# Kernel optimization log

Measured on AMD Instinct MI355X. Metric: run time of the kernel, lower is better.

Reference implementation:

```python
import jax, jax.numpy as jnp
import numpy as np

B, S, H, L, C = 32, 512, 768, 512, 3  # batch, seq, hidden, max_length, num_classes


def _lin_init(k, fan_in, shape):
    return jax.random.normal(k, shape, jnp.float32) * (1.0 / np.sqrt(fan_in))


def setup_inputs() -> dict:
    key = jax.random.key(0)
    ks = jax.random.split(key, 18)
    return {
        "tokens": jax.random.normal(ks[0], (B, S, H), jnp.float32),
        # shared Q/K/V projections (used for both token- and feature-attention)
        "Wq": _lin_init(ks[1], H, (H, H)), "bq": jnp.zeros((H,), jnp.float32),
        "Wk": _lin_init(ks[2], H, (H, H)), "bk": jnp.zeros((H,), jnp.float32),
        "Wv": _lin_init(ks[3], H, (H, H)), "bv": jnp.zeros((H,), jnp.float32),
        # TSGSA: Linear(H,1)+ReLU gate over tokens
        "W_ts": _lin_init(ks[4], H, (H, 1)), "b_ts": jnp.zeros((1,), jnp.float32),
        # FSGSA: Linear(max_length,1)+ReLU gate over padded seq axis (also reused for FGSA per source bug)
        "W_fs": _lin_init(ks[5], L, (L, 1)), "b_fs": jnp.zeros((1,), jnp.float32),
        # TGSA: Linear(H,H)+Sigmoid gate
        "W_tg": _lin_init(ks[6], H, (H, H)), "b_tg": jnp.zeros((H,), jnp.float32),
        # fnn: Linear(7H,H) -> Linear(H,C)
        "W1": _lin_init(ks[7], 7 * H, (7 * H, H)), "b1": jnp.zeros((H,), jnp.float32),
        "W2": _lin_init(ks[8], H, (H, C)), "b2": jnp.zeros((C,), jnp.float32),
    }


def _ln(x):
    # LayerNorm over (seq, hidden) jointly, eps=1e-8; freshly-instantiated affine params are identity
    m = jnp.mean(x, axis=(1, 2), keepdims=True)
    v = jnp.var(x, axis=(1, 2), keepdims=True)
    return (x - m) * jax.lax.rsqrt(v + 1e-8)


def reference(tokens, Wq, bq, Wk, bk, Wv, bv, W_ts, b_ts, W_fs, b_fs, W_tg, b_tg, W1, b1, W2, b2):
    scale = 1.0 / np.sqrt(H)
    Q = tokens @ Wq + bq  # [B,S,H]
    K = tokens @ Wk + bk
    V = tokens @ Wv + bv
    # token-direction self-attention: softmax(Q K^T / sqrt(H)) V
    att = jax.nn.softmax(jnp.einsum('bsh,bth->bst', Q, K) * scale, axis=-1)  # [B,S,S]
    TSA = jnp.einsum('bst,bth->bsh', att, V)
    # feature-direction self-attention: V @ softmax(Q^T K / sqrt(H))
    attN = jax.nn.softmax(jnp.einsum('bsh,bsg->bhg', Q, K) * scale, axis=-1)  # [B,H,H]
    FSA = jnp.einsum('bsh,bhg->bsg', V, attN)
    # gate branches
    TSGSA = jax.nn.relu(tokens @ W_ts + b_ts) * tokens  # [B,S,1]*[B,S,H]
    tpad = jnp.pad(tokens.transpose(0, 2, 1), ((0, 0), (0, 0), (0, L - S)))  # [B,H,L]
    gate_f = jax.nn.relu(tpad @ W_fs + b_fs)  # [B,H,1]
    FSGSA = (gate_f * tokens.transpose(0, 2, 1)).transpose(0, 2, 1)  # [B,S,H]
    TGSA = jax.nn.sigmoid(tokens @ W_tg + b_tg) * tokens
    FGSA = FSGSA  # source bug: FGSA branch applies self.FSGSA, identical to FSGSA
    out_all = jnp.concatenate(
        [tokens, _ln(TSA), _ln(FSA), _ln(TGSA), _ln(FGSA), _ln(TSGSA), _ln(FSGSA)], axis=2)  # [B,S,7H]
    pooled = jnp.mean(out_all, axis=1)  # [B,7H]
    return (pooled @ W1 + b1) @ W2 + b2  # [B,C]
```

## Files before the change

kernel.cpp:

```cpp
#include <hip/hip_runtime.h>
#include <cmath>

typedef unsigned short u16;
typedef __attribute__((ext_vector_type(4))) float f32x4;
typedef __attribute__((ext_vector_type(4))) unsigned int u32x4;
typedef __attribute__((ext_vector_type(8))) __bf16 bf16x8;

__device__ __forceinline__ u16 f2b(float f) {
  unsigned int u = __builtin_bit_cast(unsigned int, f);
  return (u16)((u + 0x7fffu + ((u >> 16) & 1u)) >> 16);
}
__device__ __forceinline__ float b2f(u16 h) {
  unsigned int u = ((unsigned int)h) << 16;
  return __builtin_bit_cast(float, u);
}

__device__ __forceinline__ void glds16(const u16* g, u16* l) {
  __builtin_amdgcn_global_load_lds(
      (const __attribute__((address_space(1))) void*)g,
      (__attribute__((address_space(3))) void*)l, 16, 0, 0);
}

template <int EPI>
__global__ __launch_bounds__(256) void gemm_f_k(
    const u16* __restrict__ Ap, const u16* __restrict__ Bp, u16* __restrict__ Cp,
    u16* __restrict__ CpT, const float* __restrict__ bias,
    const float* __restrict__ tokp, float* __restrict__ colsum,
    float* __restrict__ bstat, int K, int lda, int ldb, int ldc, long sA,
    long sB, long sC, float scale) {
  __shared__ alignas(16) u16 smem[4][4096];

  const int gx = gridDim.x, gxy = gx * gridDim.y;
  const int nwg = gxy * gridDim.z;
  int orig = (blockIdx.z * gridDim.y + blockIdx.y) * gx + blockIdx.x;
  int gwi = (orig & 7) * (nwg >> 3) + (orig >> 3);
  const int z = gwi / gxy;
  int rem = gwi - z * gxy;
  const int ty = rem / gx, tx = rem - ty * gx;
  const int tileM = ty << 7, tileN = tx << 7;

  const u16* Abase = Ap + (size_t)z * sA;
  const u16* Bbase = Bp + (size_t)z * sB;

  const int tid = threadIdx.x;
  const int lane = tid & 63, w = tid >> 6;
  const int wr = (w >> 1) << 6, wc = (w & 1) << 6;
  const int fr = lane & 15, fg = lane >> 4;

  f32x4 acc[4][4];
#pragma unroll
  for (int i = 0; i < 4; ++i)
#pragma unroll
    for (int j = 0; j < 4; ++j) acc[i][j] = (f32x4){0.f, 0.f, 0.f, 0.f};

  const int srow = (w << 5) + (lane >> 2), scol = (lane & 3) << 3;
  const u16* gA = Abase + (size_t)(tileM + srow) * lda + scol;
  const u16* gB = Bbase + (size_t)(tileN + srow) * ldb + scol;
  const int ldsw = (w << 5) * 32;

  auto STAGE = [&](int buf, int k0) {
    const u16* ga = gA + k0;
    const u16* gb = gB + k0;
    u16* la = &smem[buf * 2][ldsw];
    u16* lb = &smem[buf * 2 + 1][ldsw];
    glds16(ga, la);
    glds16(ga + (size_t)16 * lda, la + 512);
    glds16(gb, lb);
    glds16(gb + (size_t)16 * ldb, lb + 512);
  };

  const int nt = K >> 5;
  STAGE(0, 0);
  int cur = 0;
  for (int t = 0; t < nt; ++t) {
    if (t + 1 < nt) {
      STAGE(cur ^ 1, (t + 1) << 5);
      asm volatile("s_waitcnt vmcnt(4)" ::: "memory");
    } else {
      asm volatile("s_waitcnt vmcnt(0)" ::: "memory");
    }
    __builtin_amdgcn_s_barrier();
    asm volatile("" ::: "memory");
    const u16* Ab = smem[cur * 2];
    const u16* Bb = smem[cur * 2 + 1];
    bf16x8 av[4], bw[4];
#pragma unroll
    for (int m = 0; m < 4; ++m)
      av[m] = *(const bf16x8*)&Ab[(wr + (m << 4) + fr) * 32 + (fg << 3)];
#pragma unroll
    for (int n = 0; n < 4; ++n)
      bw[n] = *(const bf16x8*)&Bb[(wc + (n << 4) + fr) * 32 + (fg << 3)];
#pragma unroll
    for (int m = 0; m < 4; ++m)
#pragma unroll
      for (int n = 0; n < 4; ++n)
        acc[m][n] =
            __builtin_amdgcn_mfma_f32_16x16x32_bf16(av[m], bw[n], acc[m][n], 0, 0, 0);
    asm volatile("" ::: "memory");
    __builtin_amdgcn_s_barrier();
    cur ^= 1;
  }

  if constexpr (EPI == 0 || EPI == 2) {
#pragma unroll
    for (int m = 0; m < 4; ++m) {
#pragma unroll
      for (int n = 0; n < 4; ++n) {
        const int gcol = tileN + wc + (n << 4) + fr;
#pragma unroll
        for (int r = 0; r < 4; ++r) {
          const int grow = tileM + wr + (m << 4) + (fg << 2) + r;
          float v = acc[m][n][r];
          if constexpr (EPI == 0) v += bias[gcol];
          else v *= scale;
          Cp[(size_t)z * sC + (size_t)grow * ldc + gcol] = f2b(v);
        }
      }
    }
    if constexpr (EPI == 0) {
      if (CpT) {
#pragma unroll
        for (int m = 0; m < 4; ++m) {
#pragma unroll
          for (int n = 0; n < 4; ++n) {
            const int gcol = tileN + wc + (n << 4) + fr;
            const int grow0 = tileM + wr + (m << 4) + (fg << 2);
            union { u16 u[4]; unsigned long long q; } pk;
#pragma unroll
            for (int r = 0; r < 4; ++r) pk.u[r] = f2b(acc[m][n][r] + bias[gcol]);
            *(unsigned long long*)&CpT[(size_t)gcol * 16384 + grow0] = pk.q;
          }
        }
      }
    }
  } else {
    __shared__ float scol_s[128];
    __shared__ float sred[2];
    if (tid < 128) scol_s[tid] = 0.f;
    if (tid == 0) { sred[0] = 0.f; sred[1] = 0.f; }
    __syncthreads();
    float ls = 0.f, lq = 0.f;
#pragma unroll
    for (int n = 0; n < 4; ++n) {
      float cpart = 0.f;
      const int gcol = tileN + wc + (n << 4) + fr;
#pragma unroll
      for (int m = 0; m < 4; ++m) {
#pragma unroll
        for (int r = 0; r < 4; ++r) {
          float v = acc[m][n][r];
          if constexpr (EPI == 1) {
            const int grow = tileM + wr + (m << 4) + (fg << 2) + r;
            float pre = v + bias[gcol];
            float g = 1.f / (1.f + __expf(-pre));
            v = g * tokp[(size_t)grow * 768 + gcol];
          }
          cpart += v; ls += v; lq += v * v;
        }
      }
      atomicAdd(&scol_s[wc + (n << 4) + fr], cpart);
    }
    atomicAdd(&sred[0], ls);
    atomicAdd(&sred[1], lq);
    __syncthreads();
    const int b = (EPI == 1) ? (tileM >> 9) : z;
    if (tid < 128) atomicAdd(&colsum[(size_t)b * 768 + tileN + tid], scol_s[tid]);
    if (tid == 0) {
      atomicAdd(&bstat[b], sred[0]);
      atomicAdd(&bstat[32 + b], sred[1]);
    }
  }
}

__global__ __launch_bounds__(256) void cvt_tok_k(const float* __restrict__ in,
                                                 u16* __restrict__ out) {
  const size_t i = ((size_t)blockIdx.x * 256 + threadIdx.x) * 8;
  f32x4 a = *(const f32x4*)(in + i), b = *(const f32x4*)(in + i + 4);
  union { u16 u[8]; u32x4 q; } pk;
#pragma unroll
  for (int j = 0; j < 4; ++j) { pk.u[j] = f2b(a[j]); pk.u[4 + j] = f2b(b[j]); }
  *(u32x4*)(out + i) = pk.q;
}

__global__ __launch_bounds__(256) void transpose_w_k(const float* __restrict__ W,
                                                     u16* __restrict__ WT) {
  __shared__ float t[64][65];
  const int r0 = blockIdx.y << 6, c0 = blockIdx.x << 6;
  for (int i = threadIdx.x; i < 4096; i += 256) {
    int r = i >> 6, c = i & 63;
    t[r][c] = W[(size_t)(r0 + r) * 768 + c0 + c];
  }
  __syncthreads();
  for (int i = threadIdx.x; i < 4096; i += 256) {
    int rr = i >> 6, cc = i & 63;
    WT[(size_t)(c0 + rr) * 768 + r0 + cc] = f2b(t[cc][rr]);
  }
}

__global__ __launch_bounds__(256) void transpose_bf_k(const u16* __restrict__ in,
                                                      u16* __restrict__ out) {
  __shared__ u16 t[64][72];
  const size_t base = (size_t)blockIdx.z * 589824;
  const int r0 = blockIdx.y << 6, c0 = blockIdx.x << 6;
  for (int i = threadIdx.x; i < 512; i += 256) {
    int r = i >> 3, c8 = (i & 7) << 3;
    union { u32x4 q; u16 u[8]; } pk;
    pk.q = *(const u32x4*)&in[base + (size_t)(r0 + r) * 768 + c0 + c8];
#pragma unroll
    for (int j = 0; j < 8; ++j) t[c8 + j][r] = pk.u[j];
  }
  __syncthreads();
  for (int i = threadIdx.x; i < 512; i += 256) {
    int r = i >> 3, c8 = (i & 7) << 3;
    *(u32x4*)&out[base + (size_t)(c0 + r) * 768 + r0 + c8] = *(u32x4*)&t[r][c8];
  }
}

template <int LEN>
__global__ __launch_bounds__(256) void softmax_k(u16* __restrict__ data) {
  constexpr int NP = LEN / 256;
  const int row = blockIdx.x, tid = threadIdx.x;
  u16* p = data + (size_t)row * LEN;
  const int lane = tid & 63, wid = tid >> 6;
  float v[NP];
  float mx = -1e30f;
#pragma unroll
  for (int i = 0; i < NP; ++i) { v[i] = b2f(p[tid + (i << 8)]); mx = fmaxf(mx, v[i]); }
#pragma unroll
  for (int o = 32; o > 0; o >>= 1) mx = fmaxf(mx, __shfl_xor(mx, o));
  __shared__ float red[4], red2[4];
  if (lane == 0) red[wid] = mx;
  __syncthreads();
  mx = fmaxf(fmaxf(red[0], red[1]), fmaxf(red[2], red[3]));
  float sum = 0.f;
#pragma unroll
  for (int i = 0; i < NP; ++i) { v[i] = __expf(v[i] - mx); sum += v[i]; }
#pragma unroll
  for (int o = 32; o > 0; o >>= 1) sum += __shfl_xor(sum, o);
  if (lane == 0) red2[wid] = sum;
  __syncthreads();
  sum = red2[0] + red2[1] + red2[2] + red2[3];
  const float inv = 1.f / sum;
#pragma unroll
  for (int i = 0; i < NP; ++i) p[tid + (i << 8)] = f2b(v[i] * inv);
}

__global__ __launch_bounds__(256) void row_stats_k(
    const float* __restrict__ tok, const float* __restrict__ Wts,
    const float* __restrict__ bts, float* __restrict__ gate_t,
    float* __restrict__ rowsum, float* __restrict__ rowsumsq) {
  const int wid = threadIdx.x >> 6, lane = threadIdx.x & 63;
  const int row = blockIdx.x * 4 + wid;
  const float* p = tok + (size_t)row * 768;
  float s = 0.f, q = 0.f, g = 0.f;
#pragma unroll
  for (int i = 0; i < 12; ++i) {
    float t = p[lane + i * 64];
    s += t; q += t * t; g += t * Wts[lane + i * 64];
  }
#pragma unroll
  for (int o = 32; o > 0; o >>= 1) {
    s += __shfl_xor(s, o); q += __shfl_xor(q, o); g += __shfl_xor(g, o);
  }
  if (lane == 0) {
    gate_t[row] = fmaxf(g + bts[0], 0.f);
    rowsum[row] = s;
    rowsumsq[row] = q;
  }
}

__global__ __launch_bounds__(256) void col_stats_k(
    const float* __restrict__ tok, const float* __restrict__ Wfs,
    const float* __restrict__ bfs, const float* __restrict__ gate_t,
    float* __restrict__ gate_f, float* __restrict__ colsum_tok,
    float* __restrict__ colsumsq_tok, float* __restrict__ colsum_tsg) {
  const int b = blockIdx.x, h = blockIdx.y * 256 + threadIdx.x;
  const float* p = tok + (size_t)b * 512 * 768 + h;
  const float* gt = gate_t + b * 512;
  float cs = 0.f, cq = 0.f, gf = 0.f, tg = 0.f;
#pragma unroll 4
  for (int s = 0; s < 512; ++s) {
    float t = p[(size_t)s * 768];
    cs += t; cq += t * t; gf += t * Wfs[s]; tg += t * gt[s];
  }
  const int idx = b * 768 + h;
  gate_f[idx] = fmaxf(gf + bfs[0], 0.f);
  colsum_tok[idx] = cs;
  colsumsq_tok[idx] = cq;
  colsum_tsg[idx] = tg;
}

__global__ __launch_bounds__(256) void batch_stats_k(
    const float* __restrict__ gate_t, const float* __restrict__ rowsum,
    const float* __restrict__ rowsumsq, const float* __restrict__ gate_f,
    const float* __restrict__ colsum_tok, const float* __restrict__ colsumsq_tok,
    float* __restrict__ st) {
  __shared__ float red[4][256];
  const int b = blockIdx.x, tid = threadIdx.x;
  float ts = 0.f, tq = 0.f, fs = 0.f, fq = 0.f;
  for (int s = tid; s < 512; s += 256) {
    float g = gate_t[b * 512 + s];
    ts += g * rowsum[b * 512 + s];
    tq += g * g * rowsumsq[b * 512 + s];
  }
  for (int h = tid; h < 768; h += 256) {
    float g = gate_f[b * 768 + h];
    fs += g * colsum_tok[b * 768 + h];
    fq += g * g * colsumsq_tok[b * 768 + h];
  }
  red[0][tid] = ts; red[1][tid] = tq; red[2][tid] = fs; red[3][tid] = fq;
  __syncthreads();
  for (int o = 128; o > 0; o >>= 1) {
    if (tid < o) {
      red[0][tid] += red[0][tid + o];
      red[1][tid] += red[1][tid + o];
      red[2][tid] += red[2][tid + o];
      red[3][tid] += red[3][tid + o];
    }
    __syncthreads();
  }
  if (tid == 0) {
    st[b] = red[0][0]; st[32 + b] = red[1][0];
    st[64 + b] = red[2][0]; st[96 + b] = red[3][0];
  }
}

__global__ __launch_bounds__(768) void pooled_k(
    const float* __restrict__ colsum_tok, const float* __restrict__ colsum_tsa,
    const float* __restrict__ bstat_tsa, const float* __restrict__ colsum_fsa,
    const float* __restrict__ bstat_fsa, const float* __restrict__ colsum_tgsa,
    const float* __restrict__ bstat_tgsa, const float* __restrict__ colsum_tsg,
    const float* __restrict__ gate_f, const float* __restrict__ st,
    float* __restrict__ pooled) {
  const int b = blockIdx.x, h = threadIdx.x;
  const float invS = 1.f / 512.f, invN = 1.f / (512.f * 768.f);
  const int i = b * 768 + h;
  float* pr = pooled + (size_t)b * 5376;
  pr[h] = colsum_tok[i] * invS;
  auto lnslot = [&](int slot, float cs, float bs, float bq) {
    float m = bs * invN;
    float var = bq * invN - m * m;
    pr[slot * 768 + h] = (cs * invS - m) * rsqrtf(var + 1e-8f);
  };
  lnslot(1, colsum_tsa[i], bstat_tsa[b], bstat_tsa[32 + b]);
  lnslot(2, colsum_fsa[i], bstat_fsa[b], bstat_fsa[32 + b]);
  lnslot(3, colsum_tgsa[i], bstat_tgsa[b], bstat_tgsa[32 + b]);
  const float fsg_cs = gate_f[i] * colsum_tok[i];
  lnslot(4, fsg_cs, st[64 + b], st[96 + b]);
  lnslot(5, colsum_tsg[i], st[b], st[32 + b]);
  lnslot(6, fsg_cs, st[64 + b], st[96 + b]);
}

__global__ __launch_bounds__(256) void fnn1_k(const float* __restrict__ pooled,
                                              const float* __restrict__ W1,
                                              float* __restrict__ tmp1) {
  __shared__ float sp[128][36];
  const int c0 = blockIdx.x << 7, k0 = blockIdx.y << 7;
  const int tid = threadIdx.x;
  for (int i = tid; i < 4096; i += 256) {
    int b = i >> 7, j = i & 127;
    sp[j][b] = pooled[(size_t)b * 5376 + k0 + j];
  }
  __syncthreads();
  const int c = c0 + (tid & 127);
  const int u = (tid >> 7) << 4;
  float acc[16];
#pragma unroll
  for (int t = 0; t < 16; ++t) acc[t] = 0.f;
#pragma unroll 4
  for (int j = 0; j < 128; ++j) {
    float w = W1[(size_t)(k0 + j) * 768 + c];
    const f32x4* row = (const f32x4*)&sp[j][u];
#pragma unroll
    for (int t4 = 0; t4 < 4; ++t4) {
      f32x4 v = row[t4];
#pragma unroll
      for (int r = 0; r < 4; ++r) acc[t4 * 4 + r] += v[r] * w;
    }
  }
#pragma unroll
  for (int t = 0; t < 16; ++t) atomicAdd(&tmp1[(u + t) * 768 + c], acc[t]);
}

__global__ __launch_bounds__(256) void fnn2_k(const float* __restrict__ tmp1,
                                              const float* __restrict__ b1,
                                              const float* __restrict__ W2,
                                              const float* __restrict__ b2,
                                              float* __restrict__ out) {
  const int gw = blockIdx.x * 4 + (threadIdx.x >> 6);
  const int lane = threadIdx.x & 63;
  const int b = gw / 3, c = gw % 3;
  float a = 0.f;
#pragma unroll
  for (int i = 0; i < 12; ++i) {
    int k = lane + i * 64;
    a += (tmp1[b * 768 + k] + b1[k]) * W2[k * 3 + c];
  }
#pragma unroll
  for (int o = 32; o > 0; o >>= 1) a += __shfl_xor(a, o);
  if (lane == 0) out[b * 3 + c] = a + b2[c];
}

extern "C" void kernel_launch(void* const* d_in, const int* in_sizes, int n_in,
                              void* d_out, int out_size, void* d_ws, size_t ws_size,
                              hipStream_t stream) {
  const float* tokens = (const float*)d_in[0];
  const float* Wq = (const float*)d_in[1];
  const float* bq = (const float*)d_in[2];
  const float* Wk = (const float*)d_in[3];
  const float* bk = (const float*)d_in[4];
  const float* Wv = (const float*)d_in[5];
  const float* bv = (const float*)d_in[6];
  const float* Wts = (const float*)d_in[7];
  const float* bts = (const float*)d_in[8];
  const float* Wfs = (const float*)d_in[9];
  const float* bfs = (const float*)d_in[10];
  const float* Wtg = (const float*)d_in[11];
  const float* btg = (const float*)d_in[12];
  const float* W1 = (const float*)d_in[13];
  const float* b1 = (const float*)d_in[14];
  const float* W2 = (const float*)d_in[15];
  const float* b2 = (const float*)d_in[16];
  float* out = (float*)d_out;

  char* ws = (char*)d_ws;
  size_t off = 0;
  auto take = [&](size_t bytes) -> char* {
    char* p = ws + off;
    off += (bytes + 255) & ~(size_t)255;
    return p;
  };
  u16* tokb = (u16*)take((size_t)16384 * 768 * 2);
  u16* WqT = (u16*)take((size_t)768 * 768 * 2);
  u16* WkT = (u16*)take((size_t)768 * 768 * 2);
  u16* WvT = (u16*)take((size_t)768 * 768 * 2);
  u16* WtgT = (u16*)take((size_t)768 * 768 * 2);
  u16* Qb = (u16*)take((size_t)16384 * 768 * 2);
  u16* Kb = (u16*)take((size_t)16384 * 768 * 2);
  u16* Vb = (u16*)take((size_t)16384 * 768 * 2);
  u16* Qt = (u16*)take((size_t)768 * 16384 * 2);
  u16* Kt = (u16*)take((size_t)768 * 16384 * 2);
  u16* Vt = (u16*)take((size_t)768 * 16384 * 2);
  u16* attb = (u16*)take((size_t)32 * 512 * 512 * 2);
  u16* attNb = (u16*)take((size_t)32 * 768 * 768 * 2);
  u16* attNt = Qt;
  char* zbase = ws + off;
  float* colsum_tsa = (float*)take(24576 * 4);
  float* colsum_fsa = (float*)take(24576 * 4);
  float* colsum_tgsa = (float*)take(24576 * 4);
  float* bstat_tsa = (float*)take(64 * 4);
  float* bstat_fsa = (float*)take(64 * 4);
  float* bstat_tgsa = (float*)take(64 * 4);
  float* tmp1 = (float*)take((size_t)32 * 768 * 4);
  size_t zbytes = (size_t)((ws + off) - zbase);
  float* colsum_tsg = (float*)take(24576 * 4);
  float* gate_t = (float*)take(16384 * 4);
  float* rowsum = (float*)take(16384 * 4);
  float* rowsumsq = (float*)take(16384 * 4);
  float* gate_f = (float*)take(24576 * 4);
  float* colsum_tok = (float*)take(24576 * 4);
  float* colsumsq_tok = (float*)take(24576 * 4);
  float* st4 = (float*)take(128 * 4);
  float* pooled = (float*)take((size_t)32 * 5376 * 4);

  hipMemsetAsync(zbase, 0, zbytes, stream);

  const float scale = 1.0f / sqrtf(768.0f);
  const dim3 blk(256);

  cvt_tok_k<<<6144, blk, 0, stream>>>(tokens, tokb);
  transpose_w_k<<<dim3(12, 12), blk, 0, stream>>>(Wq, WqT);
  transpose_w_k<<<dim3(12, 12), blk, 0, stream>>>(Wk, WkT);
  transpose_w_k<<<dim3(12, 12), blk, 0, stream>>>(Wv, WvT);
  transpose_w_k<<<dim3(12, 12), blk, 0, stream>>>(Wtg, WtgT);

  gemm_f_k<0><<<dim3(6, 128, 1), blk, 0, stream>>>(
      tokb, WqT, Qb, Qt, bq, nullptr, nullptr, nullptr, 768, 768, 768, 768, 0,
      0, 0, 0.f);
  gemm_f_k<0><<<dim3(6, 128, 1), blk, 0, stream>>>(
      tokb, WkT, Kb, Kt, bk, nullptr, nullptr, nullptr, 768, 768, 768, 768, 0,
      0, 0, 0.f);
  gemm_f_k<0><<<dim3(6, 128, 1), blk, 0, stream>>>(
      tokb, WvT, Vb, Vt, bv, nullptr, nullptr, nullptr, 768, 768, 768, 768, 0,
      0, 0, 0.f);
  gemm_f_k<1><<<dim3(6, 128, 1), blk, 0, stream>>>(
      tokb, WtgT, nullptr, nullptr, btg, tokens, colsum_tgsa, bstat_tgsa, 768,
      768, 768, 0, 0, 0, 0, 0.f);

  gemm_f_k<2><<<dim3(6, 6, 32), blk, 0, stream>>>(
      Qt, Kt, attNb, nullptr, nullptr, nullptr, nullptr, nullptr, 512, 16384,
      16384, 768, 512, 512, 589824, scale);
  softmax_k<768><<<24576, 256, 0, stream>>>(attNb);
  transpose_bf_k<<<dim3(12, 12, 32), blk, 0, stream>>>(attNb, attNt);

  gemm_f_k<2><<<dim3(4, 4, 32), blk, 0, stream>>>(
      Qb, Kb, attb, nullptr, nullptr, nullptr, nullptr, nullptr, 768, 768, 768,
      512, 393216, 393216, 262144, scale);
  softmax_k<512><<<16384, 256, 0, stream>>>(attb);

  gemm_f_k<3><<<dim3(6, 4, 32), blk, 0, stream>>>(
      attb, Vt, nullptr, nullptr, nullptr, nullptr, colsum_tsa, bstat_tsa, 512,
      512, 16384, 0, 262144, 512, 0, 0.f);
  gemm_f_k<3><<<dim3(6, 4, 32), blk, 0, stream>>>(
      Vb, attNt, nullptr, nullptr, nullptr, nullptr, colsum_fsa, bstat_fsa, 768,
      768, 768, 0, 393216, 589824, 0, 0.f);

  row_stats_k<<<4096, blk, 0, stream>>>(tokens, Wts, bts, gate_t, rowsum, rowsumsq);
  col_stats_k<<<dim3(32, 3), blk, 0, stream>>>(tokens, Wfs, bfs, gate_t, gate_f,
                                               colsum_tok, colsumsq_tok, colsum_tsg);
  batch_stats_k<<<32, blk, 0, stream>>>(gate_t, rowsum, rowsumsq, gate_f,
                                        colsum_tok, colsumsq_tok, st4);

  pooled_k<<<32, 768, 0, stream>>>(colsum_tok, colsum_tsa, bstat_tsa, colsum_fsa,
                                   bstat_fsa, colsum_tgsa, bstat_tgsa, colsum_tsg,
                                   gate_f, st4, pooled);
  fnn1_k<<<dim3(6, 42), blk, 0, stream>>>(pooled, W1, tmp1);
  fnn2_k<<<24, blk, 0, stream>>>(tmp1, b1, W2, b2, out);
}
```

Baseline: 470.0 us.

## Fuse Q/K/V projection GEMMs into one launch and swizzle LDS tile layout

The three separate Q, K and V projection GEMMs become one launch with a grid three times wider. Each column tile picks its output buffer (Q, K or V) from its tile index, using a concatenated bias buffer and the fact that the transposed weights and the outputs sit contiguously in the workspace. The GEMM kernel also XOR-swizzles the 16-byte column chunks written to and read from LDS, to cut bank conflicts on the MFMA operand loads in every GEMM variant. In exchange, the code now depends on workspace buffers being adjacent, and the transposed-output write is unconditional for epilogue 0.

```diff
diff --git a/kernel.cpp b/kernel.cpp
--- a/kernel.cpp
+++ b/kernel.cpp
@@ -53,7 +53,8 @@
 #pragma unroll
     for (int j = 0; j < 4; ++j) acc[i][j] = (f32x4){0.f, 0.f, 0.f, 0.f};
 
-  const int srow = (w << 5) + (lane >> 2), scol = (lane & 3) << 3;
+  const int srow = (w << 5) + (lane >> 2);
+  const int scol = (((lane & 3) ^ ((lane >> 3) & 3)) << 3);
   const u16* gA = Abase + (size_t)(tileM + srow) * lda + scol;
   const u16* gB = Bbase + (size_t)(tileN + srow) * ldb + scol;
   const int ldsw = (w << 5) * 32;
@@ -69,6 +70,8 @@
     glds16(gb + (size_t)16 * ldb, lb + 512);
   };
 
+  const int col_off = ((fg ^ ((fr >> 1) & 3)) << 3);
+
   const int nt = K >> 5;
   STAGE(0, 0);
   int cur = 0;
@@ -86,10 +89,10 @@
     bf16x8 av[4], bw[4];
 #pragma unroll
     for (int m = 0; m < 4; ++m)
-      av[m] = *(const bf16x8*)&Ab[(wr + (m << 4) + fr) * 32 + (fg << 3)];
+      av[m] = *(const bf16x8*)&Ab[(wr + (m << 4) + fr) * 32 + col_off];
 #pragma unroll
     for (int n = 0; n < 4; ++n)
-      bw[n] = *(const bf16x8*)&Bb[(wc + (n << 4) + fr) * 32 + (fg << 3)];
+      bw[n] = *(const bf16x8*)&Bb[(wc + (n << 4) + fr) * 32 + col_off];
 #pragma unroll
     for (int m = 0; m < 4; ++m)
 #pragma unroll
@@ -102,34 +105,38 @@
   }
 
   if constexpr (EPI == 0 || EPI == 2) {
+    int cbuf = 0, nbase = tileN;
+    if constexpr (EPI == 0) { cbuf = tileN / 768; nbase = tileN - cbuf * 768; }
+    u16* Cz = Cp + (EPI == 0 ? (size_t)cbuf * sC : (size_t)z * sC);
 #pragma unroll
     for (int m = 0; m < 4; ++m) {
 #pragma unroll
       for (int n = 0; n < 4; ++n) {
         const int gcol = tileN + wc + (n << 4) + fr;
+        const int lcol = nbase + wc + (n << 4) + fr;
 #pragma unroll
         for (int r = 0; r < 4; ++r) {
           const int grow = tileM + wr + (m << 4) + (fg << 2) + r;
           float v = acc[m][n][r];
           if constexpr (EPI == 0) v += bias[gcol];
           else v *= scale;
-          Cp[(size_t)z * sC + (size_t)grow * ldc + gcol] = f2b(v);
+          Cz[(size_t)grow * ldc + lcol] = f2b(v);
         }
       }
     }
     if constexpr (EPI == 0) {
-      if (CpT) {
-#pragma unroll
-        for (int m = 0; m < 4; ++m) {
-#pragma unroll
-          for (int n = 0; n < 4; ++n) {
-            const int gcol = tileN + wc + (n << 4) + fr;
-            const int grow0 = tileM + wr + (m << 4) + (fg << 2);
-            union { u16 u[4]; unsigned long long q; } pk;
-#pragma unroll
-            for (int r = 0; r < 4; ++r) pk.u[r] = f2b(acc[m][n][r] + bias[gcol]);
-            *(unsigned long long*)&CpT[(size_t)gcol * 16384 + grow0] = pk.q;
-          }
+      u16* Ct = CpT + (size_t)cbuf * sC;
+#pragma unroll
+      for (int m = 0; m < 4; ++m) {
+#pragma unroll
+        for (int n = 0; n < 4; ++n) {
+          const int gcol = tileN + wc + (n << 4) + fr;
+          const int lcol = nbase + wc + (n << 4) + fr;
+          const int grow0 = tileM + wr + (m << 4) + (fg << 2);
+          union { u16 u[4]; unsigned long long q; } pk;
+#pragma unroll
+          for (int r = 0; r < 4; ++r) pk.u[r] = f2b(acc[m][n][r] + bias[gcol]);
+          *(unsigned long long*)&Ct[(size_t)lcol * 16384 + grow0] = pk.q;
         }
       }
     }
@@ -444,6 +451,7 @@
   u16* attb = (u16*)take((size_t)32 * 512 * 512 * 2);
   u16* attNb = (u16*)take((size_t)32 * 768 * 768 * 2);
   u16* attNt = Qt;
+  float* bias3 = (float*)take(2304 * 4);
   char* zbase = ws + off;
   float* colsum_tsa = (float*)take(24576 * 4);
   float* colsum_fsa = (float*)take(24576 * 4);
@@ -464,6 +472,9 @@
   float* pooled = (float*)take((size_t)32 * 5376 * 4);
 
   hipMemsetAsync(zbase, 0, zbytes, stream);
+  hipMemcpyAsync(bias3, bq, 768 * 4, hipMemcpyDeviceToDevice, stream);
+  hipMemcpyAsync(bias3 + 768, bk, 768 * 4, hipMemcpyDeviceToDevice, stream);
+  hipMemcpyAsync(bias3 + 1536, bv, 768 * 4, hipMemcpyDeviceToDevice, stream);
 
   const float scale = 1.0f / sqrtf(768.0f);
   const dim3 blk(256);
@@ -474,15 +485,9 @@
   transpose_w_k<<<dim3(12, 12), blk, 0, stream>>>(Wv, WvT);
   transpose_w_k<<<dim3(12, 12), blk, 0, stream>>>(Wtg, WtgT);
 
-  gemm_f_k<0><<<dim3(6, 128, 1), blk, 0, stream>>>(
-      tokb, WqT, Qb, Qt, bq, nullptr, nullptr, nullptr, 768, 768, 768, 768, 0,
-      0, 0, 0.f);
-  gemm_f_k<0><<<dim3(6, 128, 1), blk, 0, stream>>>(
-      tokb, WkT, Kb, Kt, bk, nullptr, nullptr, nullptr, 768, 768, 768, 768, 0,
-      0, 0, 0.f);
-  gemm_f_k<0><<<dim3(6, 128, 1), blk, 0, stream>>>(
-      tokb, WvT, Vb, Vt, bv, nullptr, nullptr, nullptr, 768, 768, 768, 768, 0,
-      0, 0, 0.f);
+  gemm_f_k<0><<<dim3(18, 128, 1), blk, 0, stream>>>(
+      tokb, WqT, Qb, Qt, bias3, nullptr, nullptr, nullptr, 768, 768, 768, 768,
+      0, 0, 12582912, 0.f);
   gemm_f_k<1><<<dim3(6, 128, 1), blk, 0, stream>>>(
       tokb, WtgT, nullptr, nullptr, btg, tokens, colsum_tgsa, bstat_tgsa, 768,
       768, 768, 0, 0, 0, 0, 0.f);
```

Measured after the change: 464.3 us. About the same (-1.2%).
